# Kernel optimization log

Measured on AMD Instinct MI355X. Metric: run time of the kernel, lower is better.

Reference implementation:

```python
import jax, jax.numpy as jnp
import numpy as np

B, S, D = 2, 2048, 1024
H = 16
HD = D // H  # 64
SCALE = HD ** -0.5
EPS = 1e-12  # F.normalize eps


def _rope_sin_cos(length, half, dtype):
    positions = jnp.arange(length, dtype=dtype)
    freqs = jnp.arange(half, dtype=dtype)
    inv_freq = 1.0 / 10000 ** (freqs / max(1, half))
    theta = jnp.einsum('s,f->sf', positions, inv_freq)  # [S, half]
    return jnp.sin(theta)[None, None], jnp.cos(theta)[None, None]  # [1,1,S,half]


def _rotate(x, sin, cos):
    # x: [B,H,S,HD]; interleaved even/odd rotation
    x_even = x[..., 0::2]
    x_odd = x[..., 1::2]
    r_even = x_even * cos - x_odd * sin
    r_odd = x_even * sin + x_odd * cos
    return jnp.stack([r_even, r_odd], axis=-1).reshape(x.shape)


def setup_inputs() -> dict:
    key = jax.random.key(0)
    k1, k2, k3 = jax.random.split(key, 3)
    tokens = jax.random.normal(k1, (B, S, D), dtype=jnp.float32)
    qkv_w = jax.random.normal(k2, (3 * D, D), dtype=jnp.float32) * (D ** -0.5)
    qkv_b = jnp.zeros((3 * D,), dtype=jnp.float32)
    out_w = jax.random.normal(k3, (D, D), dtype=jnp.float32) * (D ** -0.5)
    out_b = jnp.zeros((D,), dtype=jnp.float32)
    return {"tokens": tokens, "qkv_w": qkv_w, "qkv_b": qkv_b,
            "out_w": out_w, "out_b": out_b}


def reference(tokens, qkv_w, qkv_b, out_w, out_b):
    batch, length, _ = tokens.shape
    qkv = tokens @ qkv_w.T + qkv_b                       # [B,S,3D]
    qkv = qkv.reshape(batch, length, 3, H, HD)
    qkv = jnp.transpose(qkv, (0, 3, 1, 2, 4))            # [B,H,S,3,HD]
    q, k, v = qkv[..., 0, :], qkv[..., 1, :], qkv[..., 2, :]
    sin, cos = _rope_sin_cos(length, HD // 2, q.dtype)
    q = _rotate(q, sin, cos)
    k = _rotate(k, sin, cos)
    # QK L2-normalize (F.normalize: x / max(||x||, eps))
    q = q / jnp.maximum(jnp.linalg.norm(q, axis=-1, keepdims=True), EPS)
    k = k / jnp.maximum(jnp.linalg.norm(k, axis=-1, keepdims=True), EPS)
    scores = jnp.einsum('bhqd,bhkd->bhqk', q, k) * SCALE
    attn = jax.nn.softmax(scores, axis=-1)
    out = jnp.einsum('bhqk,bhkd->bhqd', attn, v)          # [B,H,S,HD]
    out = jnp.transpose(out, (0, 2, 1, 3)).reshape(batch, length, D)
    return out @ out_w.T + out_b
```

## Files before the change

kernel.cpp:

```cpp
#include <hip/hip_runtime.h>
#include <hip/hip_bf16.h>
#include <math.h>

#define B_ 2
#define S_ 2048
#define D_ 1024
#define H_ 16
#define HD_ 64
#define BHS (B_*H_*S_)
#define NROWS (B_*S_)

typedef __attribute__((ext_vector_type(8))) short bf16x8;
typedef __attribute__((ext_vector_type(4))) short bf16x4;
typedef __attribute__((ext_vector_type(4))) float f32x4;
typedef __attribute__((ext_vector_type(4))) int i32x4;

#ifdef __HIP_DEVICE_COMPILE__
#define EXP2(x) __builtin_amdgcn_exp2f(x)
#else
#define EXP2(x) exp2f(x)
#endif

#define MFMA32(a, b, c) __builtin_amdgcn_mfma_f32_16x16x32_bf16(a, b, c, 0, 0, 0)

#define SCALE_LOG2E 0.18033688011112043f

__device__ __forceinline__ short f2bf(float x) {
  __hip_bfloat16 h = __float2bfloat16(x);
  return *reinterpret_cast<short*>(&h);
}
__device__ __forceinline__ int packbf_hu(float lo, float hi) {
  unsigned lb = __float_as_uint(lo) + 0x8000u;
  unsigned hb = __float_as_uint(hi) + 0x8000u;
  return (int)__builtin_amdgcn_perm(hb, lb, 0x07060302u);
}

__device__ __forceinline__ void gload_lds16(const short* g, short* l) {
  __builtin_amdgcn_global_load_lds(
      (const __attribute__((address_space(1))) void*)g,
      (__attribute__((address_space(3))) void*)l, 16, 0, 0);
}

__global__ __launch_bounds__(256) void prep(
    const float* __restrict__ tokens, const float* __restrict__ qkv_w,
    const float* __restrict__ out_w, short* __restrict__ tok_bf,
    short* __restrict__ qkvw_bf, short* __restrict__ outw_bf,
    float* __restrict__ tab) {
  const int i = blockIdx.x * 256 + threadIdx.x;
  const float* src;
  short* dst;
  int j;
  if (i < 524288) {
    src = tokens; dst = tok_bf; j = i;
  } else if (i < 917504) {
    src = qkv_w; dst = qkvw_bf; j = i - 524288;
  } else if (i < 1048576) {
    src = out_w; dst = outw_bf; j = i - 917504;
  } else if (i < 1056768) {
    const int e = (i - 1048576) * 8;
    const int s = e >> 5;
    const int f0 = e & 31;
#pragma unroll
    for (int k = 0; k < 8; k++) {
      const int f = f0 + k;
      const float theta = (float)s * exp2f(-(float)f * 0.41524101186092034f);
      float sn, cs;
      sincosf(theta, &sn, &cs);
      tab[(s * 32 + f) * 2] = sn;
      tab[(s * 32 + f) * 2 + 1] = cs;
    }
    return;
  } else {
    return;
  }
  const float4 a = *(const float4*)(src + (long)j * 8);
  const float4 b = *(const float4*)(src + (long)j * 8 + 4);
  short tmp[8] = {f2bf(a.x), f2bf(a.y), f2bf(a.z), f2bf(a.w),
                  f2bf(b.x), f2bf(b.y), f2bf(b.z), f2bf(b.w)};
  *(bf16x8*)(dst + (long)j * 8) = *(const bf16x8*)tmp;
}

__global__ __launch_bounds__(256) void qkv_mfma(
    const short* __restrict__ A, const short* __restrict__ W,
    const float* __restrict__ bias, const float* __restrict__ tab,
    short* __restrict__ qb, short* __restrict__ kb, short* __restrict__ vtb) {
  __shared__ short smem[16384];
  const int t = threadIdx.x;
  const int w = t >> 6;
  const int lane = t & 63;
  const int col = lane & 15;
  const int quad = lane >> 4;
  const int wm = w >> 1;
  const int wn = w & 1;
  const int bid = blockIdx.x;
  const int xcd = bid & 7;
  const int seq = bid >> 3;
  const int m0 = (seq / 3) * 128;
  const int n0 = (xcd * 3 + seq % 3) * 128;

  f32x4 acc[4][4] = {};

  auto stage = [&](short* As, short* Bs, int k0) {
#pragma unroll
    for (int i = 0; i < 2; i++) {
      const int c0 = i * 256 + w * 64;
      const int c = c0 + lane;
      const int row = c >> 2;
      const int gseg = (c & 3) ^ ((row >> 1) & 3);
      gload_lds16(&A[(m0 + row) * 1024 + k0 + gseg * 8], As + c0 * 8);
    }
#pragma unroll
    for (int i = 0; i < 2; i++) {
      const int c0 = i * 256 + w * 64;
      const int c = c0 + lane;
      const int row = c >> 2;
      const int gseg = (c & 3) ^ ((row >> 1) & 3);
      gload_lds16(&W[(n0 + row) * 1024 + k0 + gseg * 8], Bs + c0 * 8);
    }
  };

  auto compute = [&](const short* As, const short* Bs) {
    bf16x8 af[4], bfr[4];
#pragma unroll
    for (int mt = 0; mt < 4; mt++) {
      const int m = wm * 64 + mt * 16 + col;
      af[mt] = *(const bf16x8*)&As[m * 32 + ((quad ^ ((m >> 1) & 3)) * 8)];
    }
#pragma unroll
    for (int nt = 0; nt < 4; nt++) {
      const int n = wn * 64 + nt * 16 + col;
      bfr[nt] = *(const bf16x8*)&Bs[n * 32 + ((quad ^ ((n >> 1) & 3)) * 8)];
    }
#pragma unroll
    for (int mt = 0; mt < 4; mt++)
#pragma unroll
      for (int nt = 0; nt < 4; nt++)
        acc[mt][nt] = MFMA32(af[mt], bfr[nt], acc[mt][nt]);
  };

  short* As0 = smem;
  short* Bs0 = smem + 4096;
  short* As1 = smem + 8192;
  short* Bs1 = smem + 12288;

  stage(As0, Bs0, 0);
  __syncthreads();
  for (int it = 0; it < 16; it++) {
    const int k0 = it * 64;
    stage(As1, Bs1, k0 + 32);
    compute(As0, Bs0);
    __syncthreads();
    if (it < 15) stage(As0, Bs0, k0 + 64);
    compute(As1, Bs1);
    __syncthreads();
  }

  const int j_base = n0 + wn * 64;
  const int c = j_base >> 10;
  const int h = (j_base >> 6) & 15;
  float bi[4];
#pragma unroll
  for (int nt = 0; nt < 4; nt++) bi[nt] = bias[j_base + nt * 16 + col];

  if (c < 2) {
    short* dst = (c == 0) ? qb : kb;
    float* Tf = (float*)smem + w * 1088;
#pragma unroll
    for (int mt = 0; mt < 4; mt++) {
#pragma unroll
      for (int nt = 0; nt < 4; nt++)
#pragma unroll
        for (int r = 0; r < 4; r++)
          Tf[(quad * 4 + r) * 68 + nt * 16 + col] = acc[mt][nt][r] + bi[nt];
#pragma unroll
      for (int p = 0; p < 4; p++) {
        const int rloc = p * 4 + quad;
        const int n = m0 + wm * 64 + mt * 16 + rloc;
        const int bidx = n >> 11;
        const int s = n & 2047;
        const float4 xv = *(const float4*)&Tf[rloc * 68 + col * 4];
        const float4 tc = *(const float4*)&tab[s * 64 + col * 4];
        const float e0 = xv.x * tc.y - xv.y * tc.x;
        const float o0 = xv.x * tc.x + xv.y * tc.y;
        const float e1 = xv.z * tc.w - xv.w * tc.z;
        const float o1 = xv.z * tc.z + xv.w * tc.w;
        float ss = e0 * e0 + o0 * o0 + e1 * e1 + o1 * o1;
        ss += __shfl_xor(ss, 1, 64);
        ss += __shfl_xor(ss, 2, 64);
        ss += __shfl_xor(ss, 4, 64);
        ss += __shfl_xor(ss, 8, 64);
        const float scl = 1.0f / fmaxf(sqrtf(ss), 1e-12f);
        int2 pk;
        pk.x = packbf_hu(e0 * scl, o0 * scl);
        pk.y = packbf_hu(e1 * scl, o1 * scl);
        *(int2*)&dst[((long)(bidx * 16 + h) * 2048 + s) * 64 + col * 4] = pk;
      }
    }
  } else {
    const int bidx = m0 >> 11;
    const int st = ((m0 & 2047) >> 6) + wm;
    short* vbase = vtb + ((long)(bidx * 16 + h) * 32 + st) * 4096;
#pragma unroll
    for (int mt = 0; mt < 4; mt++)
#pragma unroll
      for (int ntq = 0; ntq < 4; ntq++) {
        int2 pk;
        pk.x = packbf_hu(acc[mt][ntq][0] + bi[ntq], acc[mt][ntq][1] + bi[ntq]);
        pk.y = packbf_hu(acc[mt][ntq][2] + bi[ntq], acc[mt][ntq][3] + bi[ntq]);
        *(int2*)&vbase[((mt * 4 + ntq) * 32 + quad * 8 + (col >> 1)) * 8 +
                       (col & 1) * 4] = pk;
      }
  }
}

__global__ __launch_bounds__(512) void attn_mfma(
    const short* __restrict__ qb,
    const short* __restrict__ kb,
    const short* __restrict__ vt,
    short* __restrict__ ob) {
  __shared__ __align__(16) char smem[65536];
  short* Ks = (short*)smem;
  short* Vs = Ks + 16384;
  const int t = threadIdx.x;
  const int w = t >> 6;
  const int grp = w >> 2;
  const int wl = w & 3;
  const int lane = t & 63;
  const int col = lane & 15;
  const int quad = lane >> 4;
  const int bh = blockIdx.x;
  const int q0 = blockIdx.y * 128;
  const long hb = (long)bh * S_ * 64;
  const short* kg = kb + hb;
  const short* vg = vt + (long)bh * 64 * S_;

  bf16x8 qa[2][2];
#pragma unroll
  for (int mt2 = 0; mt2 < 2; mt2++)
#pragma unroll
    for (int h = 0; h < 2; h++)
      qa[mt2][h] = *(const bf16x8*)&qb[hb +
          (long)(q0 + wl * 32 + mt2 * 16 + col) * 64 + h * 32 + quad * 8];

  const int tt = (wl << 6) | lane;
  int kofs[2];
#pragma unroll
  for (int i = 0; i < 2; i++) {
    const int cc = tt + 256 * i;
    kofs[i] = ((cc >> 7) * 16 + (cc & 15)) * 64 + ((cc >> 6) & 1) * 32 +
              ((cc >> 4) & 3) * 8;
  }

  short* KfL0 = Ks + grp * 4096;
  short* KfL1 = KfL0 + 8192;
  short* VfL0 = Vs + grp * 4096;
  short* VfL1 = VfL0 + 8192;

  f32x4 oacc[2][4] = {};
  f32x4 lacc[2] = {};
  const short oneb = 0x3F80;
  const bf16x8 ones8 = {oneb, oneb, oneb, oneb, oneb, oneb, oneb, oneb};

  auto stage = [&](short* KfL, short* VfL, int kt) {
    const short* kgp = kg + (long)kt * 64;
    const short* vgp = vg + (long)(kt >> 6) * 4096;
#pragma unroll
    for (int i = 0; i < 2; i++) {
      gload_lds16(kgp + kofs[i], KfL + i * 2048 + wl * 512);
      gload_lds16(vgp + (tt + 256 * i) * 8, VfL + i * 2048 + wl * 512);
    }
  };

  auto compute = [&](const short* KfL, const short* VfL) {
#pragma unroll
    for (int ntp = 0; ntp < 2; ntp++) {
      i32x4 pw[2];
#pragma unroll
      for (int half = 0; half < 2; half++) {
        const int nt = ntp * 2 + half;
        const bf16x8 ka0 =
            *(const bf16x8*)&KfL[nt * 1024 + quad * 128 + col * 8];
        const bf16x8 ka1 =
            *(const bf16x8*)&KfL[nt * 1024 + 512 + quad * 128 + col * 8];
#pragma unroll
        for (int mt2 = 0; mt2 < 2; mt2++) {
          f32x4 z = {0.f, 0.f, 0.f, 0.f};
          z = MFMA32(ka0, qa[mt2][0], z);
          z = MFMA32(ka1, qa[mt2][1], z);
          const float e0 = EXP2(z[0] * SCALE_LOG2E);
          const float e1 = EXP2(z[1] * SCALE_LOG2E);
          const float e2 = EXP2(z[2] * SCALE_LOG2E);
          const float e3 = EXP2(z[3] * SCALE_LOG2E);
          if (half == 0) {
            pw[mt2].x = packbf_hu(e0, e1);
            pw[mt2].y = packbf_hu(e2, e3);
          } else {
            pw[mt2].z = packbf_hu(e0, e1);
            pw[mt2].w = packbf_hu(e2, e3);
          }
        }
      }
      const bf16x8 pb0 = __builtin_bit_cast(bf16x8, pw[0]);
      const bf16x8 pb1 = __builtin_bit_cast(bf16x8, pw[1]);
      lacc[0] = MFMA32(ones8, pb0, lacc[0]);
      lacc[1] = MFMA32(ones8, pb1, lacc[1]);
#pragma unroll
      for (int dt = 0; dt < 4; dt++) {
        const bf16x4 v0 = *(const bf16x4*)
            &VfL[((ntp * 2 + 0) * 4 + dt) * 256 + quad * 64 + col * 4];
        const bf16x4 v1 = *(const bf16x4*)
            &VfL[((ntp * 2 + 1) * 4 + dt) * 256 + quad * 64 + col * 4];
        const bf16x8 va = __builtin_shufflevector(v0, v1, 0, 1, 2, 3, 4, 5, 6, 7);
        oacc[0][dt] = MFMA32(va, pb0, oacc[0][dt]);
        oacc[1][dt] = MFMA32(va, pb1, oacc[1][dt]);
      }
    }
  };

  const int base = grp * 1024;
  stage(KfL0, VfL0, base);
  __syncthreads();
  for (int it = 0; it < 8; it++) {
    const int kt0 = base + it * 128;
    stage(KfL1, VfL1, kt0 + 64);
    compute(KfL0, VfL0);
    __syncthreads();
    if (it < 7) stage(KfL0, VfL0, kt0 + 128);
    compute(KfL1, VfL1);
    __syncthreads();
  }

  float* Ocomb = (float*)smem;
  float* lsumC = (float*)(smem + 34816);
  if (grp == 1) {
#pragma unroll
    for (int mt2 = 0; mt2 < 2; mt2++) {
      const int qloc = wl * 32 + mt2 * 16 + col;
      if (quad == 0) lsumC[qloc] = lacc[mt2][0];
#pragma unroll
      for (int dt = 0; dt < 4; dt++)
        *(f32x4*)&Ocomb[qloc * 68 + dt * 16 + quad * 4] = oacc[mt2][dt];
    }
  }
  __syncthreads();
  if (grp == 0) {
#pragma unroll
    for (int mt2 = 0; mt2 < 2; mt2++) {
      const int qloc = wl * 32 + mt2 * 16 + col;
      const float inv = 1.0f / (lacc[mt2][0] + lsumC[qloc]);
      short* orow = ob + hb + (long)(q0 + qloc) * 64;
#pragma unroll
      for (int dt = 0; dt < 4; dt++) {
        const float4 oc = *(const float4*)&Ocomb[qloc * 68 + dt * 16 + quad * 4];
        int2 pk;
        pk.x = packbf_hu((oacc[mt2][dt][0] + oc.x) * inv,
                         (oacc[mt2][dt][1] + oc.y) * inv);
        pk.y = packbf_hu((oacc[mt2][dt][2] + oc.z) * inv,
                         (oacc[mt2][dt][3] + oc.w) * inv);
        *(int2*)&orow[dt * 16 + quad * 4] = pk;
      }
    }
  }
}

__global__ __launch_bounds__(256) void out_mfma(
    const short* __restrict__ O, const short* __restrict__ W,
    const float* __restrict__ bias, float* __restrict__ out) {
  __shared__ short smem[8192];
  const int t = threadIdx.x;
  const int w = t >> 6;
  const int lane = t & 63;
  const int col = lane & 15;
  const int quad = lane >> 4;
  const int wm = w >> 1;
  const int wn = w & 1;
  const int bid = blockIdx.x;
  const int xcd = bid & 7;
  const int seq = bid >> 3;
  const int m0 = (seq >> 1) * 64;
  const int n0 = (xcd * 2 + (seq & 1)) * 64;

  f32x4 acc[2][2] = {};

  auto stage = [&](short* As, short* Bs, int k0) {
    {
      const int c = w * 64 + lane;
      const int row = c >> 2;
      const int gseg = (c & 3) ^ ((row >> 1) & 3);
      const int n = m0 + row;
      const int bidx = n >> 11;
      const int s = n & 2047;
      const int kk = k0 + gseg * 8;
      gload_lds16(&O[((long)(bidx * 16 + (kk >> 6)) * 2048 + s) * 64 + (kk & 63)],
                  As + w * 512);
    }
    {
      const int c = w * 64 + lane;
      const int row = c >> 2;
      const int gseg = (c & 3) ^ ((row >> 1) & 3);
      gload_lds16(&W[(n0 + row) * 1024 + k0 + gseg * 8], Bs + w * 512);
    }
  };

  auto compute = [&](const short* As, const short* Bs) {
    bf16x8 af[2], bfr[2];
#pragma unroll
    for (int mt = 0; mt < 2; mt++) {
      const int m = wm * 32 + mt * 16 + col;
      af[mt] = *(const bf16x8*)&As[m * 32 + ((quad ^ ((m >> 1) & 3)) * 8)];
    }
#pragma unroll
    for (int nt = 0; nt < 2; nt++) {
      const int n = wn * 32 + nt * 16 + col;
      bfr[nt] = *(const bf16x8*)&Bs[n * 32 + ((quad ^ ((n >> 1) & 3)) * 8)];
    }
#pragma unroll
    for (int mt = 0; mt < 2; mt++)
#pragma unroll
      for (int nt = 0; nt < 2; nt++)
        acc[mt][nt] = MFMA32(af[mt], bfr[nt], acc[mt][nt]);
  };

  short* As0 = smem;
  short* Bs0 = smem + 2048;
  short* As1 = smem + 4096;
  short* Bs1 = smem + 6144;

  stage(As0, Bs0, 0);
  __syncthreads();
  for (int it = 0; it < 16; it++) {
    const int k0 = it * 64;
    stage(As1, Bs1, k0 + 32);
    compute(As0, Bs0);
    __syncthreads();
    if (it < 15) stage(As0, Bs0, k0 + 64);
    compute(As1, Bs1);
    __syncthreads();
  }

  float bi[2];
#pragma unroll
  for (int nt = 0; nt < 2; nt++) bi[nt] = bias[n0 + wn * 32 + nt * 16 + col];
#pragma unroll
  for (int mt = 0; mt < 2; mt++) {
#pragma unroll
    for (int r = 0; r < 4; r++) {
      const int n = m0 + wm * 32 + mt * 16 + quad * 4 + r;
#pragma unroll
      for (int nt = 0; nt < 2; nt++)
        out[(long)n * 1024 + n0 + wn * 32 + nt * 16 + col] =
            acc[mt][nt][r] + bi[nt];
    }
  }
}

extern "C" void kernel_launch(void* const* d_in, const int* in_sizes, int n_in,
                              void* d_out, int out_size, void* d_ws,
                              size_t ws_size, hipStream_t stream) {
  const float* tokens = (const float*)d_in[0];
  const float* qkv_w = (const float*)d_in[1];
  const float* qkv_b = (const float*)d_in[2];
  const float* out_w = (const float*)d_in[3];
  const float* out_b = (const float*)d_in[4];
  float* out = (float*)d_out;

  const size_t per = (size_t)BHS * HD_;
  float* tab = (float*)d_ws;
  short* tok_bf = (short*)(tab + 2048 * 64);
  short* qkvw_bf = tok_bf + per;
  short* outw_bf = qkvw_bf + 3 * per / 4;
  short* q_bf = outw_bf + per / 4;
  short* k_bf = q_bf + per;
  short* vt_bf = k_bf + per;
  short* O_bf = vt_bf + per;

  hipLaunchKernelGGL(prep, dim3(4128), dim3(256), 0, stream, tokens, qkv_w,
                     out_w, tok_bf, qkvw_bf, outw_bf, tab);
  hipLaunchKernelGGL(qkv_mfma, dim3(768), dim3(256), 0, stream, tok_bf,
                     qkvw_bf, qkv_b, tab, q_bf, k_bf, vt_bf);
  hipLaunchKernelGGL(attn_mfma, dim3(B_ * H_, S_ / 128), dim3(512), 0, stream,
                     q_bf, k_bf, vt_bf, O_bf);
  hipLaunchKernelGGL(out_mfma, dim3(1024), dim3(256), 0, stream, O_bf,
                     outw_bf, out_b, out);
}
```

Measured before the change: 184.4 us.

## Triple-buffer GEMM K-loop with vmcnt waits, fold softmax scale into Q, widen V layout

Both projection GEMMs switch from double buffering with full __syncthreads to a three-stage LDS ring. Each step uses explicit s_waitcnt vmcnt plus a raw barrier, so two tiles' global-to-LDS loads stay in flight while one tile is computed. The attention scale times log2e is folded into the normalized Q at write time, which removes a multiply per score before exp2. The V-transpose output layout is also changed so attention reads one 16-byte vector instead of two 8-byte loads, with matching 16-byte stores in the QKV epilogue. The cost is more LDS per block, and correctness depends on the hand-set vmcnt counts matching the loads issued per stage.

```diff
diff --git a/kernel.cpp b/kernel.cpp
--- a/kernel.cpp
+++ b/kernel.cpp
@@ -24,6 +24,10 @@
 #define MFMA32(a, b, c) __builtin_amdgcn_mfma_f32_16x16x32_bf16(a, b, c, 0, 0, 0)
 
 #define SCALE_LOG2E 0.18033688011112043f
+
+#define VMCNT(N) asm volatile("s_waitcnt vmcnt(" #N ")" ::: "memory")
+#define SBAR() do { __builtin_amdgcn_s_barrier(); \
+                    __builtin_amdgcn_sched_barrier(0); } while (0)
 
 __device__ __forceinline__ short f2bf(float x) {
   __hip_bfloat16 h = __float2bfloat16(x);
@@ -84,7 +88,7 @@
     const short* __restrict__ A, const short* __restrict__ W,
     const float* __restrict__ bias, const float* __restrict__ tab,
     short* __restrict__ qb, short* __restrict__ kb, short* __restrict__ vtb) {
-  __shared__ short smem[16384];
+  __shared__ short smem[24576];
   const int t = threadIdx.x;
   const int w = t >> 6;
   const int lane = t & 63;
@@ -138,22 +142,21 @@
         acc[mt][nt] = MFMA32(af[mt], bfr[nt], acc[mt][nt]);
   };
 
-  short* As0 = smem;
-  short* Bs0 = smem + 4096;
-  short* As1 = smem + 8192;
-  short* Bs1 = smem + 12288;
+  short* As0 = smem;          short* Bs0 = smem + 4096;
+  short* As1 = smem + 8192;   short* Bs1 = smem + 12288;
+  short* As2 = smem + 16384;  short* Bs2 = smem + 20480;
 
   stage(As0, Bs0, 0);
+  stage(As1, Bs1, 32);
+  for (int it = 0; it < 10; it++) {
+    const int k = it * 96;
+    VMCNT(4); SBAR(); stage(As2, Bs2, k + 64);  compute(As0, Bs0);
+    VMCNT(4); SBAR(); stage(As0, Bs0, k + 96);  compute(As1, Bs1);
+    VMCNT(4); SBAR(); stage(As1, Bs1, k + 128); compute(As2, Bs2);
+  }
+  VMCNT(4); SBAR(); compute(As0, Bs0);
+  VMCNT(0); SBAR(); compute(As1, Bs1);
   __syncthreads();
-  for (int it = 0; it < 16; it++) {
-    const int k0 = it * 64;
-    stage(As1, Bs1, k0 + 32);
-    compute(As0, Bs0);
-    __syncthreads();
-    if (it < 15) stage(As0, Bs0, k0 + 64);
-    compute(As1, Bs1);
-    __syncthreads();
-  }
 
   const int j_base = n0 + wn * 64;
   const int c = j_base >> 10;
@@ -189,7 +192,8 @@
         ss += __shfl_xor(ss, 2, 64);
         ss += __shfl_xor(ss, 4, 64);
         ss += __shfl_xor(ss, 8, 64);
-        const float scl = 1.0f / fmaxf(sqrtf(ss), 1e-12f);
+        float scl = 1.0f / fmaxf(sqrtf(ss), 1e-12f);
+        if (c == 0) scl *= SCALE_LOG2E;
         int2 pk;
         pk.x = packbf_hu(e0 * scl, o0 * scl);
         pk.y = packbf_hu(e1 * scl, o1 * scl);
@@ -201,14 +205,19 @@
     const int st = ((m0 & 2047) >> 6) + wm;
     short* vbase = vtb + ((long)(bidx * 16 + h) * 32 + st) * 4096;
 #pragma unroll
-    for (int mt = 0; mt < 4; mt++)
+    for (int mtp = 0; mtp < 2; mtp++)
 #pragma unroll
       for (int ntq = 0; ntq < 4; ntq++) {
-        int2 pk;
-        pk.x = packbf_hu(acc[mt][ntq][0] + bi[ntq], acc[mt][ntq][1] + bi[ntq]);
-        pk.y = packbf_hu(acc[mt][ntq][2] + bi[ntq], acc[mt][ntq][3] + bi[ntq]);
-        *(int2*)&vbase[((mt * 4 + ntq) * 32 + quad * 8 + (col >> 1)) * 8 +
-                       (col & 1) * 4] = pk;
+        int4 pk4;
+        pk4.x = packbf_hu(acc[2 * mtp][ntq][0] + bi[ntq],
+                          acc[2 * mtp][ntq][1] + bi[ntq]);
+        pk4.y = packbf_hu(acc[2 * mtp][ntq][2] + bi[ntq],
+                          acc[2 * mtp][ntq][3] + bi[ntq]);
+        pk4.z = packbf_hu(acc[2 * mtp + 1][ntq][0] + bi[ntq],
+                          acc[2 * mtp + 1][ntq][1] + bi[ntq]);
+        pk4.w = packbf_hu(acc[2 * mtp + 1][ntq][2] + bi[ntq],
+                          acc[2 * mtp + 1][ntq][3] + bi[ntq]);
+        *(int4*)&vbase[(mtp * 4 + ntq) * 512 + quad * 128 + col * 8] = pk4;
       }
   }
 }
@@ -287,10 +296,10 @@
           f32x4 z = {0.f, 0.f, 0.f, 0.f};
           z = MFMA32(ka0, qa[mt2][0], z);
           z = MFMA32(ka1, qa[mt2][1], z);
-          const float e0 = EXP2(z[0] * SCALE_LOG2E);
-          const float e1 = EXP2(z[1] * SCALE_LOG2E);
-          const float e2 = EXP2(z[2] * SCALE_LOG2E);
-          const float e3 = EXP2(z[3] * SCALE_LOG2E);
+          const float e0 = EXP2(z[0]);
+          const float e1 = EXP2(z[1]);
+          const float e2 = EXP2(z[2]);
+          const float e3 = EXP2(z[3]);
           if (half == 0) {
             pw[mt2].x = packbf_hu(e0, e1);
             pw[mt2].y = packbf_hu(e2, e3);
@@ -306,11 +315,8 @@
       lacc[1] = MFMA32(ones8, pb1, lacc[1]);
 #pragma unroll
       for (int dt = 0; dt < 4; dt++) {
-        const bf16x4 v0 = *(const bf16x4*)
-            &VfL[((ntp * 2 + 0) * 4 + dt) * 256 + quad * 64 + col * 4];
-        const bf16x4 v1 = *(const bf16x4*)
-            &VfL[((ntp * 2 + 1) * 4 + dt) * 256 + quad * 64 + col * 4];
-        const bf16x8 va = __builtin_shufflevector(v0, v1, 0, 1, 2, 3, 4, 5, 6, 7);
+        const bf16x8 va = *(const bf16x8*)
+            &VfL[(ntp * 4 + dt) * 512 + quad * 128 + col * 8];
         oacc[0][dt] = MFMA32(va, pb0, oacc[0][dt]);
         oacc[1][dt] = MFMA32(va, pb1, oacc[1][dt]);
       }
@@ -366,7 +372,7 @@
 __global__ __launch_bounds__(256) void out_mfma(
     const short* __restrict__ O, const short* __restrict__ W,
     const float* __restrict__ bias, float* __restrict__ out) {
-  __shared__ short smem[8192];
+  __shared__ short smem[12288];
   const int t = threadIdx.x;
   const int w = t >> 6;
   const int lane = t & 63;
@@ -421,22 +427,20 @@
         acc[mt][nt] = MFMA32(af[mt], bfr[nt], acc[mt][nt]);
   };
 
-  short* As0 = smem;
-  short* Bs0 = smem + 2048;
-  short* As1 = smem + 4096;
-  short* Bs1 = smem + 6144;
+  short* As0 = smem;          short* Bs0 = smem + 2048;
+  short* As1 = smem + 4096;   short* Bs1 = smem + 6144;
+  short* As2 = smem + 8192;   short* Bs2 = smem + 10240;
 
   stage(As0, Bs0, 0);
-  __syncthreads();
-  for (int it = 0; it < 16; it++) {
-    const int k0 = it * 64;
-    stage(As1, Bs1, k0 + 32);
-    compute(As0, Bs0);
-    __syncthreads();
-    if (it < 15) stage(As0, Bs0, k0 + 64);
-    compute(As1, Bs1);
-    __syncthreads();
-  }
+  stage(As1, Bs1, 32);
+  for (int it = 0; it < 10; it++) {
+    const int k = it * 96;
+    VMCNT(2); SBAR(); stage(As2, Bs2, k + 64);  compute(As0, Bs0);
+    VMCNT(2); SBAR(); stage(As0, Bs0, k + 96);  compute(As1, Bs1);
+    VMCNT(2); SBAR(); stage(As1, Bs1, k + 128); compute(As2, Bs2);
+  }
+  VMCNT(2); SBAR(); compute(As0, Bs0);
+  VMCNT(0); SBAR(); compute(As1, Bs1);
 
   float bi[2];
 #pragma unroll
```

Result: faster. 180.8 us (-2.0%).
